# Optimization experiments

Hardware: AMD Instinct MI355X
Metric: run time of the kernel (lower is better)

Reference implementation:

```python
import jax, jax.numpy as jnp
import numpy as np

B, T, D_MODEL, WINDOW = 2, 2048, 512, 32


def setup_inputs() -> dict:
    key = jax.random.key(0)
    ks = jax.random.split(key, 5)
    s = 1.0 / np.sqrt(D_MODEL)
    x = jax.random.normal(ks[0], (B, T, D_MODEL), jnp.float32)
    # torch.nn.Linear convention: weight [out_features, in_features], y = x @ W.T + b
    w_qkv = jax.random.uniform(ks[1], (3 * D_MODEL, D_MODEL), jnp.float32, -s, s)
    b_qkv = jax.random.uniform(ks[2], (3 * D_MODEL,), jnp.float32, -s, s)
    w_proj = jax.random.uniform(ks[3], (D_MODEL, D_MODEL), jnp.float32, -s, s)
    b_proj = jax.random.uniform(ks[4], (D_MODEL,), jnp.float32, -s, s)
    return {"x": x, "w_qkv": w_qkv, "b_qkv": b_qkv, "w_proj": w_proj, "b_proj": b_proj}


def reference(x, w_qkv, b_qkv, w_proj, b_proj):
    Bb, Tt, C = x.shape
    qkv = x @ w_qkv.T + b_qkv                      # [B,T,3C]
    q, k, v = jnp.split(qkv, 3, axis=-1)           # each [B,T,C]
    W = 2 * WINDOW - 1                             # non-causal window span [t-w+1, t+w-1]
    offs = jnp.arange(W) - (WINDOW - 1)            # [W]
    idx = jnp.arange(Tt)[:, None] + offs[None, :]  # [T,W] absolute key positions
    valid = (idx >= 0) & (idx < Tt)                # mask out-of-range window slots
    idx_c = jnp.clip(idx, 0, Tt - 1)
    k_win = k[:, idx_c]                            # [B,T,W,C]
    v_win = v[:, idx_c]                            # [B,T,W,C]
    scale = jnp.asarray(C, x.dtype) ** 0.5
    scores = jnp.einsum('btc,btwc->btw', q, k_win) / scale
    scores = jnp.where(valid[None], scores, -jnp.inf)
    p = jax.nn.softmax(scores, axis=-1)            # [B,T,W]
    out = jnp.einsum('btw,btwc->btc', p, v_win)    # [B,T,C]
    return out @ w_proj.T + b_proj
```

## Files before the change

kernel.cpp:

```cpp
#include <hip/hip_runtime.h>
#include <math.h>

#define BB 2
#define TT 2048
#define CC 512
#define WIN 32
#define WSZ 63
#define MM (BB * TT)

typedef __attribute__((ext_vector_type(8))) short short8;
typedef __attribute__((ext_vector_type(4))) float floatx4;

__device__ inline unsigned short bf16_rn(float f) {
  unsigned u = __builtin_bit_cast(unsigned, f);
  u += 0x7fff + ((u >> 16) & 1);
  return (unsigned short)(u >> 16);
}
__device__ inline unsigned pack_bf16x2(float lo, float hi) {
  return (unsigned)bf16_rn(lo) | ((unsigned)bf16_rn(hi) << 16);
}

#define NX  (MM * CC)
#define NWQ (3 * CC * CC)
#define NWP (CC * CC)

__global__ __launch_bounds__(256) void convert_bf16(
    const float* __restrict__ x, const float* __restrict__ wq,
    const float* __restrict__ wp, ushort* __restrict__ xb,
    ushort* __restrict__ wqb, ushort* __restrict__ wpb) {
  const size_t e = ((size_t)blockIdx.x * 256 + threadIdx.x) * 8;
  const float* src;
  ushort* dst;
  size_t off;
  if (e < NX) {
    const size_t m = e >> 9, k = e & 511;
    src = x + e; dst = xb;
    off = (m >> 4) * 8192 + (k >> 3) * 128 + (m & 15) * 8;
  } else if (e < NX + NWQ) {
    src = wq; dst = wqb; off = e - NX; src += off;
  } else {
    src = wp; dst = wpb; off = e - NX - NWQ; src += off;
  }
  float4 v0 = ((const float4*)src)[0];
  float4 v1 = ((const float4*)src)[1];
  uint4 o;
  o.x = pack_bf16x2(v0.x, v0.y);
  o.y = pack_bf16x2(v0.z, v0.w);
  o.z = pack_bf16x2(v1.x, v1.y);
  o.w = pack_bf16x2(v1.z, v1.w);
  *(uint4*)(dst + off) = o;
}

#define PSTR 264
#define VSTR 136

template <int BM, bool ATILED, typename OT>
__global__ __launch_bounds__(256) void gemm_panel(
    const ushort* __restrict__ A, const ushort* __restrict__ B,
    const float* __restrict__ bias, OT* __restrict__ C,
    ushort* __restrict__ VT, int M, int N) {
  constexpr int MIW = BM / 64;
  __shared__ __align__(16) ushort Bs[64 * PSTR];

  const int tid = threadIdx.x;
  const int lane = tid & 63;
  const int wave = tid >> 6;
  const int m0 = blockIdx.y * BM;
  const int n0 = blockIdx.x * 64;
  const int wm = wave * (BM / 4);
  const int mlane = lane & 15, quad = lane >> 4;

  floatx4 acc[MIW][4];
#pragma unroll
  for (int i = 0; i < MIW; ++i)
#pragma unroll
    for (int j = 0; j < 4; ++j) acc[i][j] = (floatx4){0.f, 0.f, 0.f, 0.f};

  for (int h = 0; h < 2; ++h) {
    if (h) __syncthreads();
#pragma unroll
    for (int i = 0; i < 8; ++i) {
      const int idx = tid + 256 * i;
      const int r = idx >> 5, kc = (idx & 31) * 8;
      *(uint4*)(&Bs[r * PSTR + kc]) =
          *(const uint4*)(B + (size_t)(n0 + r) * CC + h * 256 + kc);
    }
    __syncthreads();
#pragma unroll
    for (int ks = 0; ks < 8; ++ks) {
      short8 bfr[4];
#pragma unroll
      for (int ni = 0; ni < 4; ++ni)
        bfr[ni] = *(const short8*)(&Bs[(ni * 16 + mlane) * PSTR + ks * 32 + quad * 8]);
#pragma unroll
      for (int mi = 0; mi < MIW; ++mi) {
        short8 af;
        if constexpr (ATILED) {
          af = *(const short8*)(
              A + (size_t)((m0 + wm) / 16 + mi) * 8192 +
                  (size_t)(h * 32 + ks * 4 + quad) * 128 + mlane * 8);
        } else {
          af = *(const short8*)(
              A + (size_t)(m0 + wm + mi * 16 + mlane) * CC + h * 256 + ks * 32 + quad * 8);
        }
#pragma unroll
        for (int ni = 0; ni < 4; ++ni)
          acc[mi][ni] = __builtin_amdgcn_mfma_f32_16x16x32_bf16(af, bfr[ni], acc[mi][ni], 0, 0, 0);
      }
    }
  }

  const bool vpath = (VT != nullptr) && (n0 >= 1024);
  if (!vpath) {
#pragma unroll
    for (int ni = 0; ni < 4; ++ni) {
      const int n = n0 + ni * 16 + mlane;
      const float bn = bias[n];
#pragma unroll
      for (int mi = 0; mi < MIW; ++mi) {
        const int mbase = m0 + wm + mi * 16 + quad * 4;
#pragma unroll
        for (int r = 0; r < 4; ++r) {
          float val = acc[mi][ni][r] + bn;
          if constexpr (sizeof(OT) == 2)
            ((ushort*)C)[(size_t)(mbase + r) * N + n] = bf16_rn(val);
          else
            ((float*)C)[(size_t)(mbase + r) * N + n] = val;
        }
      }
    }
  } else if constexpr (BM == 128) {
    ushort* Vt = Bs;
    __syncthreads();
#pragma unroll
    for (int ni = 0; ni < 4; ++ni) {
      const int n_l = ni * 16 + mlane;
      const float bn = bias[n0 + n_l];
#pragma unroll
      for (int mi = 0; mi < MIW; ++mi) {
        const int m_l = wm + mi * 16 + quad * 4;
        ushort4 pk;
        pk.x = bf16_rn(acc[mi][ni][0] + bn);
        pk.y = bf16_rn(acc[mi][ni][1] + bn);
        pk.z = bf16_rn(acc[mi][ni][2] + bn);
        pk.w = bf16_rn(acc[mi][ni][3] + bn);
        *(ushort4*)(&Vt[n_l * VSTR + m_l]) = pk;
      }
    }
    __syncthreads();
#pragma unroll
    for (int i = 0; i < 4; ++i) {
      const int idx = tid + 256 * i;
      const int n_l = idx >> 4, mo = (idx & 15) * 8;
      *(uint4*)(VT + (size_t)(n0 - 1024 + n_l) * M + m0 + mo) =
          *(const uint4*)(&Vt[n_l * VSTR + mo]);
    }
  }
}

#define ATILE 16
#define SLD 84
#define PLD 104

__global__ __launch_bounds__(256) void attn_mfma(
    const ushort* __restrict__ qkv, const ushort* __restrict__ vT,
    ushort* __restrict__ out) {
  __shared__ __align__(16) float s_s[16 * SLD];
  __shared__ __align__(16) ushort p_s[16 * PLD];

  const int tid = threadIdx.x;
  const int wave = tid >> 6, lane = tid & 63;
  const int mlane = lane & 15, quad = lane >> 4;
  const int tile = ((blockIdx.x & 7) << 5) | (blockIdx.x >> 3);
  const int bt0 = tile * ATILE;
  const int b = bt0 / TT, t0 = bt0 % TT;
  const ushort* qbase = qkv + (size_t)b * TT * (3 * CC);

  const ushort* qrow  = qbase + (ptrdiff_t)(t0 + mlane) * (3 * CC);
  const ushort* krow0 = qbase + (ptrdiff_t)(t0 - 32 + wave * 16 + mlane) * (3 * CC) + CC;
  const ushort* krow1 = qbase + (ptrdiff_t)(t0 - 32 + 64 + mlane) * (3 * CC) + CC;
  floatx4 sacc0 = (floatx4){0.f, 0.f, 0.f, 0.f};
  floatx4 sacc1 = (floatx4){0.f, 0.f, 0.f, 0.f};
#pragma unroll
  for (int ks = 0; ks < 16; ++ks) {
    short8 a  = *(const short8*)(qrow + ks * 32 + quad * 8);
    short8 b0 = *(const short8*)(krow0 + ks * 32 + quad * 8);
    sacc0 = __builtin_amdgcn_mfma_f32_16x16x32_bf16(a, b0, sacc0, 0, 0, 0);
    if (wave == 0) {
      short8 b1 = *(const short8*)(krow1 + ks * 32 + quad * 8);
      sacc1 = __builtin_amdgcn_mfma_f32_16x16x32_bf16(a, b1, sacc1, 0, 0, 0);
    }
  }

#pragma unroll
  for (int r = 0; r < 4; ++r)
    s_s[(quad * 4 + r) * SLD + wave * 16 + mlane] = sacc0[r];
  if (wave == 0) {
#pragma unroll
    for (int r = 0; r < 4; ++r)
      s_s[(quad * 4 + r) * SLD + 64 + mlane] = sacc1[r];
  }
  __syncthreads();

  {
    const int row = tid >> 4, li = tid & 15;
    const float inv_scale = 0.044194173824159216f;
    float e[5];
    float mx = -INFINITY;
#pragma unroll
    for (int i = 0; i < 5; ++i) {
      const int r = li + 16 * i;
      const int j = r - 1 - row;
      const int src = t0 - 32 + r;
      const bool valid = (j >= 0) && (j < WSZ) && (src >= 0) && (src < TT);
      e[i] = valid ? s_s[row * SLD + r] * inv_scale : -INFINITY;
      mx = fmaxf(mx, e[i]);
    }
    mx = fmaxf(mx, __shfl_xor(mx, 1)); mx = fmaxf(mx, __shfl_xor(mx, 2));
    mx = fmaxf(mx, __shfl_xor(mx, 4)); mx = fmaxf(mx, __shfl_xor(mx, 8));
    float sum = 0.f;
#pragma unroll
    for (int i = 0; i < 5; ++i) {
      e[i] = (e[i] == -INFINITY) ? 0.f : __expf(e[i] - mx);
      sum += e[i];
    }
    sum += __shfl_xor(sum, 1); sum += __shfl_xor(sum, 2);
    sum += __shfl_xor(sum, 4); sum += __shfl_xor(sum, 8);
    const float rs = 1.f / sum;
#pragma unroll
    for (int i = 0; i < 5; ++i)
      p_s[row * PLD + li + 16 * i] = bf16_rn(e[i] * rs);
    if (li < 8) {
      p_s[row * PLD + 80 + li] = 0;
      p_s[row * PLD + 88 + li] = 0;
      p_s[row * PLD + 96 + li] = 0;
    }
  }
  __syncthreads();

  short8 pa[3];
#pragma unroll
  for (int ks = 0; ks < 3; ++ks)
    pa[ks] = *(const short8*)(&p_s[mlane * PLD + ks * 32 + quad * 8]);

  const ptrdiff_t mcol0 = (ptrdiff_t)b * TT + t0 - 32;
#pragma unroll 2
  for (int nt8 = 0; nt8 < 8; ++nt8) {
    const int nt = wave * 8 + nt8;
    const ushort* vrow = vT + (ptrdiff_t)(nt * 16 + mlane) * MM + mcol0;
    floatx4 o = (floatx4){0.f, 0.f, 0.f, 0.f};
#pragma unroll
    for (int ks = 0; ks < 3; ++ks) {
      short8 bv = *(const short8*)(vrow + ks * 32 + quad * 8);
      o = __builtin_amdgcn_mfma_f32_16x16x32_bf16(pa[ks], bv, o, 0, 0, 0);
    }
#pragma unroll
    for (int r = 0; r < 4; ++r)
      out[(size_t)(bt0 + quad * 4 + r) * CC + nt * 16 + mlane] = bf16_rn(o[r]);
  }
}

extern "C" void kernel_launch(void* const* d_in, const int* in_sizes, int n_in,
                              void* d_out, int out_size, void* d_ws, size_t ws_size,
                              hipStream_t stream) {
  const float* x      = (const float*)d_in[0];
  const float* w_qkv  = (const float*)d_in[1];
  const float* b_qkv  = (const float*)d_in[2];
  const float* w_proj = (const float*)d_in[3];
  const float* b_proj = (const float*)d_in[4];
  float* outp = (float*)d_out;

  ushort* base  = (ushort*)d_ws;
  ushort* qkv   = base + 131072;
  ushort* attn  = qkv + (size_t)MM * 3 * CC;
  ushort* xb    = attn + (size_t)MM * CC;
  ushort* wqb   = xb + (size_t)NX;
  ushort* wpb   = wqb + (size_t)NWQ;
  ushort* vTg   = wpb + (size_t)NWP;
  ushort* vT    = vTg + 64;

  convert_bf16<<<(NX + NWQ + NWP) / (256 * 8), 256, 0, stream>>>(x, w_qkv, w_proj, xb, wqb, wpb);
  {
    dim3 grid((3 * CC) / 64, MM / 128);
    gemm_panel<128, true, ushort><<<grid, 256, 0, stream>>>(xb, wqb, b_qkv, qkv, vT, MM, 3 * CC);
  }
  attn_mfma<<<MM / ATILE, 256, 0, stream>>>(qkv, vT, attn);
  {
    dim3 grid(CC / 64, MM / 64);
    gemm_panel<64, false, float><<<grid, 256, 0, stream>>>(attn, wpb, b_proj, outp, nullptr, MM, CC);
  }
}
```

Before: 104.5 us.

## Store Q and K in MFMA-tiled layout for contiguous attention fragment loads

The QKV GEMM epilogue now writes Q and K into separate buffers laid out in 16-row MFMA fragment tiles instead of a row-major interleaved qkv buffer. The attention kernel then reads its Q and K fragments as contiguous 16-byte chunks within each 8192-element tile rather than strided rows of width 3C. This is meant to improve the coalescing of attention loads. The cost is scattered 2-byte stores in the GEMM epilogue, which may slow the QKV GEMM. Negative tile indices at sequence edges rely on the existing workspace padding before the buffers.

```diff
diff --git a/kernel.cpp b/kernel.cpp
--- a/kernel.cpp
+++ b/kernel.cpp
@@ -54,7 +54,7 @@
 #define PSTR 264
 #define VSTR 136
 
-template <int BM, bool ATILED, typename OT>
+template <int BM, bool ATILED, bool QKT, typename OT>
 __global__ __launch_bounds__(256) void gemm_panel(
     const ushort* __restrict__ A, const ushort* __restrict__ B,
     const float* __restrict__ bias, OT* __restrict__ C,
@@ -110,8 +110,52 @@
     }
   }
 
-  const bool vpath = (VT != nullptr) && (n0 >= 1024);
-  if (!vpath) {
+  if constexpr (QKT) {
+    if (n0 < 1024) {
+      ushort* dst = (ushort*)C + (n0 < 512 ? 0 : 2097152);
+      const int c0 = n0 & 511;
+#pragma unroll
+      for (int ni = 0; ni < 4; ++ni) {
+        const int c = c0 + ni * 16 + mlane;
+        const float bn = bias[n0 + ni * 16 + mlane];
+        const int kpo = (c >> 3) * 128 + (c & 7);
+#pragma unroll
+        for (int mi = 0; mi < MIW; ++mi) {
+          const size_t mb =
+              (size_t)((m0 + wm) / 16 + mi) * 8192 + kpo + (size_t)quad * 32;
+#pragma unroll
+          for (int r = 0; r < 4; ++r)
+            dst[mb + r * 8] = bf16_rn(acc[mi][ni][r] + bn);
+        }
+      }
+    } else if constexpr (BM == 128) {
+      ushort* Vt = Bs;
+      __syncthreads();
+#pragma unroll
+      for (int ni = 0; ni < 4; ++ni) {
+        const int n_l = ni * 16 + mlane;
+        const float bn = bias[n0 + n_l];
+#pragma unroll
+        for (int mi = 0; mi < MIW; ++mi) {
+          const int m_l = wm + mi * 16 + quad * 4;
+          ushort4 pk;
+          pk.x = bf16_rn(acc[mi][ni][0] + bn);
+          pk.y = bf16_rn(acc[mi][ni][1] + bn);
+          pk.z = bf16_rn(acc[mi][ni][2] + bn);
+          pk.w = bf16_rn(acc[mi][ni][3] + bn);
+          *(ushort4*)(&Vt[n_l * VSTR + m_l]) = pk;
+        }
+      }
+      __syncthreads();
+#pragma unroll
+      for (int i = 0; i < 4; ++i) {
+        const int idx = tid + 256 * i;
+        const int n_l = idx >> 4, mo = (idx & 15) * 8;
+        *(uint4*)(VT + (size_t)(n0 - 1024 + n_l) * M + m0 + mo) =
+            *(const uint4*)(&Vt[n_l * VSTR + mo]);
+      }
+    }
+  } else {
 #pragma unroll
     for (int ni = 0; ni < 4; ++ni) {
       const int n = n0 + ni * 16 + mlane;
@@ -129,32 +173,6 @@
         }
       }
     }
-  } else if constexpr (BM == 128) {
-    ushort* Vt = Bs;
-    __syncthreads();
-#pragma unroll
-    for (int ni = 0; ni < 4; ++ni) {
-      const int n_l = ni * 16 + mlane;
-      const float bn = bias[n0 + n_l];
-#pragma unroll
-      for (int mi = 0; mi < MIW; ++mi) {
-        const int m_l = wm + mi * 16 + quad * 4;
-        ushort4 pk;
-        pk.x = bf16_rn(acc[mi][ni][0] + bn);
-        pk.y = bf16_rn(acc[mi][ni][1] + bn);
-        pk.z = bf16_rn(acc[mi][ni][2] + bn);
-        pk.w = bf16_rn(acc[mi][ni][3] + bn);
-        *(ushort4*)(&Vt[n_l * VSTR + m_l]) = pk;
-      }
-    }
-    __syncthreads();
-#pragma unroll
-    for (int i = 0; i < 4; ++i) {
-      const int idx = tid + 256 * i;
-      const int n_l = idx >> 4, mo = (idx & 15) * 8;
-      *(uint4*)(VT + (size_t)(n0 - 1024 + n_l) * M + m0 + mo) =
-          *(const uint4*)(&Vt[n_l * VSTR + mo]);
-    }
   }
 }
 
@@ -163,8 +181,8 @@
 #define PLD 104
 
 __global__ __launch_bounds__(256) void attn_mfma(
-    const ushort* __restrict__ qkv, const ushort* __restrict__ vT,
-    ushort* __restrict__ out) {
+    const ushort* __restrict__ Qb, const ushort* __restrict__ Kb,
+    const ushort* __restrict__ vT, ushort* __restrict__ out) {
   __shared__ __align__(16) float s_s[16 * SLD];
   __shared__ __align__(16) ushort p_s[16 * PLD];
 
@@ -174,20 +192,19 @@
   const int tile = ((blockIdx.x & 7) << 5) | (blockIdx.x >> 3);
   const int bt0 = tile * ATILE;
   const int b = bt0 / TT, t0 = bt0 % TT;
-  const ushort* qbase = qkv + (size_t)b * TT * (3 * CC);
-
-  const ushort* qrow  = qbase + (ptrdiff_t)(t0 + mlane) * (3 * CC);
-  const ushort* krow0 = qbase + (ptrdiff_t)(t0 - 32 + wave * 16 + mlane) * (3 * CC) + CC;
-  const ushort* krow1 = qbase + (ptrdiff_t)(t0 - 32 + 64 + mlane) * (3 * CC) + CC;
+
+  const ushort* qp  = Qb + (size_t)tile * 8192 + quad * 128 + mlane * 8;
+  const ushort* kp0 = Kb + (ptrdiff_t)(tile - 2 + wave) * 8192 + quad * 128 + mlane * 8;
+  const ushort* kp1 = Kb + (ptrdiff_t)(tile + 2) * 8192 + quad * 128 + mlane * 8;
   floatx4 sacc0 = (floatx4){0.f, 0.f, 0.f, 0.f};
   floatx4 sacc1 = (floatx4){0.f, 0.f, 0.f, 0.f};
 #pragma unroll
   for (int ks = 0; ks < 16; ++ks) {
-    short8 a  = *(const short8*)(qrow + ks * 32 + quad * 8);
-    short8 b0 = *(const short8*)(krow0 + ks * 32 + quad * 8);
+    short8 a  = *(const short8*)(qp + ks * 512);
+    short8 b0 = *(const short8*)(kp0 + ks * 512);
     sacc0 = __builtin_amdgcn_mfma_f32_16x16x32_bf16(a, b0, sacc0, 0, 0, 0);
     if (wave == 0) {
-      short8 b1 = *(const short8*)(krow1 + ks * 32 + quad * 8);
+      short8 b1 = *(const short8*)(kp1 + ks * 512);
       sacc1 = __builtin_amdgcn_mfma_f32_16x16x32_bf16(a, b1, sacc1, 0, 0, 0);
     }
   }
@@ -271,9 +288,10 @@
   float* outp = (float*)d_out;
 
   ushort* base  = (ushort*)d_ws;
-  ushort* qkv   = base + 131072;
-  ushort* attn  = qkv + (size_t)MM * 3 * CC;
-  ushort* xb    = attn + (size_t)MM * CC;
+  ushort* Qb    = base + 131072;
+  ushort* Kb    = Qb + 2097152;
+  ushort* attn  = Kb + 2097152;
+  ushort* xb    = attn + 2097152;
   ushort* wqb   = xb + (size_t)NX;
   ushort* wpb   = wqb + (size_t)NWQ;
   ushort* vTg   = wpb + (size_t)NWP;
@@ -282,11 +300,13 @@
   convert_bf16<<<(NX + NWQ + NWP) / (256 * 8), 256, 0, stream>>>(x, w_qkv, w_proj, xb, wqb, wpb);
   {
     dim3 grid((3 * CC) / 64, MM / 128);
-    gemm_panel<128, true, ushort><<<grid, 256, 0, stream>>>(xb, wqb, b_qkv, qkv, vT, MM, 3 * CC);
-  }
-  attn_mfma<<<MM / ATILE, 256, 0, stream>>>(qkv, vT, attn);
+    gemm_panel<128, true, true, ushort><<<grid, 256, 0, stream>>>(
+        xb, wqb, b_qkv, Qb, vT, MM, 3 * CC);
+  }
+  attn_mfma<<<MM / ATILE, 256, 0, stream>>>(Qb, Kb, vT, attn);
   {
     dim3 grid(CC / 64, MM / 64);
-    gemm_panel<64, false, float><<<grid, 256, 0, stream>>>(attn, wpb, b_proj, outp, nullptr, MM, CC);
-  }
-}
+    gemm_panel<64, false, false, float><<<grid, 256, 0, stream>>>(
+        attn, wpb, b_proj, outp, nullptr, MM, CC);
+  }
+}
```

Result: no change. 104.4 us (-0.1%).
